# Kernel tuning notes

Measured on AMD Instinct MI355X. Metric: run time of the kernel, lower is better.

Reference implementation:

```python
import jax, jax.numpy as jnp
import numpy as np

B = 4096
N_ENTITY = 100000
N_USER = 10000
N_RELATION = 32
DIM = 64
N_ITER = 2
K = 16  # n_neighbors


def setup_inputs() -> dict:
    key = jax.random.key(0)
    ks = jax.random.split(key, 8)
    pairs = jax.random.randint(ks[0], (B, 2), 0, N_USER, dtype=jnp.int64 if jax.config.jax_enable_x64 else jnp.int32)
    adj_entity = jax.random.randint(ks[1], (N_ENTITY, K), 0, N_ENTITY)
    adj_relation = jax.random.randint(ks[2], (N_ENTITY, K), 0, N_RELATION)
    # xavier_uniform-style scale for embeddings
    def xavier(k, shape):
        limit = float(np.sqrt(6.0 / (shape[0] + shape[1])))
        return jax.random.uniform(k, shape, jnp.float32, -limit, limit)
    entity_emb = xavier(ks[3], (N_ENTITY, DIM))
    relation_emb = xavier(ks[4], (N_RELATION, DIM))
    user_emb = xavier(ks[5], (N_USER, DIM))
    W = xavier(ks[6], (DIM, DIM))
    b = jnp.zeros((DIM,), jnp.float32)
    return {"pairs": pairs, "adj_entity": adj_entity, "adj_relation": adj_relation,
            "entity_emb": entity_emb, "relation_emb": relation_emb,
            "user_emb": user_emb, "W": W, "b": b}


def reference(pairs, adj_entity, adj_relation, entity_emb, relation_emb, user_emb, W, b):
    n = pairs.shape[0]
    dim = entity_emb.shape[1]
    k = adj_entity.shape[1]
    users = pairs[:, 0]
    items = pairs[:, 1]

    # multi-hop neighbor expansion (mirrors get_neighbors)
    entities = [items]
    relations = []
    for i in range(N_ITER):
        entities.append(adj_entity[entities[i]].reshape(-1))
        relations.append(adj_relation[entities[i]].reshape(-1))

    u = user_emb[users]  # [B, D]
    ev = [entity_emb[entities[i]].reshape(n, -1, dim) for i in range(N_ITER + 1)]
    rv = [relation_emb[relations[i]].reshape(n, -1, dim) for i in range(N_ITER)]

    for l in range(N_ITER):
        nxt = []
        for i in range(N_ITER - l):
            r = rv[i].reshape(n, -1, k, dim)          # [B, M, K, D]
            scores = jnp.einsum('bd,bmkd->bmk', u, r) # user-relation attention
            attn = jax.nn.softmax(scores, axis=-1)[..., None]
            nbr = (attn * ev[i + 1].reshape(n, -1, k, dim)).sum(axis=-2)  # [B, M, D]
            x = ev[i].reshape(n, -1, dim) + nbr       # residual add
            h = x @ W.T + b                            # Linear(dim, dim)
            nxt.append(jnp.tanh(h) if l == N_ITER - 1 else jax.nn.relu(h))
        ev = nxt

    item_embeddings = ev[0].reshape(-1, dim)  # [B, D]
    return jax.nn.sigmoid(jnp.sum(u * item_embeddings, axis=1))
```

## Files before the change

kernel.cpp:

```cpp
#include <hip/hip_runtime.h>
#include <hip/hip_bf16.h>
#include <math.h>

#define DIM  64
#define KN   16
#define NREL 32
#define S8   0.00390625f

__device__ __forceinline__ float frcp(float x) { return __builtin_amdgcn_rcpf(x); }

__device__ __forceinline__ unsigned short f2bf(float f) {
    unsigned u = __float_as_uint(f);
    u = (u + 0x7fffu + ((u >> 16) & 1u)) >> 16;
    return (unsigned short)u;
}

typedef __attribute__((ext_vector_type(8))) short bfrag;
typedef __attribute__((ext_vector_type(4))) float f32x4;
typedef __attribute__((ext_vector_type(2))) float f32x2;

__global__ __launch_bounds__(256, 2) void we_kernel_mfma(
    const float* __restrict__ entity_emb,
    const float* __restrict__ W,
    const int* __restrict__ adjE,
    const int* __restrict__ adjR,
    unsigned char* __restrict__ WE8,
    int* __restrict__ adjP,
    int nRows)
{
    const int tid  = threadIdx.x;
    const int wave = tid >> 6;
    const int lane = tid & 63;
    const int c = lane & 15;
    const int g = lane >> 4;

    {
        const size_t nEntries = (size_t)nRows * KN;
        const size_t base = ((size_t)blockIdx.x * 256 + tid) * 8;
        if (base + 8 <= nEntries) {
            const int4* e4 = (const int4*)(adjE + base);
            const int4* r4 = (const int4*)(adjR + base);
            const int4 e0 = e4[0], e1v = e4[1];
            const int4 r0 = r4[0], r1v = r4[1];
            int4 p0, p1;
            p0.x = (e0.x << 5) | r0.x;  p0.y = (e0.y << 5) | r0.y;
            p0.z = (e0.z << 5) | r0.z;  p0.w = (e0.w << 5) | r0.w;
            p1.x = (e1v.x << 5) | r1v.x; p1.y = (e1v.y << 5) | r1v.y;
            p1.z = (e1v.z << 5) | r1v.z; p1.w = (e1v.w << 5) | r1v.w;
            ((int4*)(adjP + base))[0] = p0;
            ((int4*)(adjP + base))[1] = p1;
        } else if (base < nEntries) {
            for (size_t i = base; i < nEntries; ++i)
                adjP[i] = (adjE[i] << 5) | adjR[i];
        }
    }

    const int nTiles = (nRows + 15) >> 4;
    const int t0 = (blockIdx.x * 4 + wave) * 2;
    if (t0 >= nTiles) return;

    bfrag a[4][2];
    #pragma unroll
    for (int m = 0; m < 4; ++m) {
        #pragma unroll
        for (int ks = 0; ks < 2; ++ks) {
            const float4* ws = (const float4*)(W + (size_t)(16 * m + c) * DIM + 8 * g + 32 * ks);
            const float4 w0 = ws[0], w1 = ws[1];
            a[m][ks][0] = (short)f2bf(w0.x); a[m][ks][1] = (short)f2bf(w0.y);
            a[m][ks][2] = (short)f2bf(w0.z); a[m][ks][3] = (short)f2bf(w0.w);
            a[m][ks][4] = (short)f2bf(w1.x); a[m][ks][5] = (short)f2bf(w1.y);
            a[m][ks][6] = (short)f2bf(w1.z); a[m][ks][7] = (short)f2bf(w1.w);
        }
    }

    float4 pe[2][4];
    #pragma unroll
    for (int j = 0; j < 2; ++j) {
        const int t = (t0 + j < nTiles) ? (t0 + j) : 0;
        int row = 16 * t + c;
        if (row >= nRows) row = nRows - 1;
        const float4* src = (const float4*)(entity_emb + (size_t)row * DIM + 8 * g);
        pe[j][0] = src[0];
        pe[j][1] = src[1];
        pe[j][2] = src[8];
        pe[j][3] = src[9];
    }

    #pragma unroll
    for (int j = 0; j < 2; ++j) {
        const int t = t0 + j;
        if (t >= nTiles) continue;

        bfrag b0, b1;
        b0[0] = (short)f2bf(pe[j][0].x); b0[1] = (short)f2bf(pe[j][0].y);
        b0[2] = (short)f2bf(pe[j][0].z); b0[3] = (short)f2bf(pe[j][0].w);
        b0[4] = (short)f2bf(pe[j][1].x); b0[5] = (short)f2bf(pe[j][1].y);
        b0[6] = (short)f2bf(pe[j][1].z); b0[7] = (short)f2bf(pe[j][1].w);
        b1[0] = (short)f2bf(pe[j][2].x); b1[1] = (short)f2bf(pe[j][2].y);
        b1[2] = (short)f2bf(pe[j][2].z); b1[3] = (short)f2bf(pe[j][2].w);
        b1[4] = (short)f2bf(pe[j][3].x); b1[5] = (short)f2bf(pe[j][3].y);
        b1[6] = (short)f2bf(pe[j][3].z); b1[7] = (short)f2bf(pe[j][3].w);

        f32x4 acc[4];
        #pragma unroll
        for (int m = 0; m < 4; ++m) {
            f32x4 z = {0.f, 0.f, 0.f, 0.f};
            z = __builtin_amdgcn_mfma_f32_16x16x32_bf16(a[m][0], b0, z, 0, 0, 0);
            z = __builtin_amdgcn_mfma_f32_16x16x32_bf16(a[m][1], b1, z, 0, 0, 0);
            acc[m] = z;
        }

        const int erow = 16 * t + c;
        if (erow < nRows) {
            #pragma unroll
            for (int m = 0; m < 4; ++m) {
                int r8 = 0;
                r8 = __builtin_amdgcn_cvt_pk_fp8_f32(acc[m][0] * 256.f, acc[m][1] * 256.f, r8, false);
                r8 = __builtin_amdgcn_cvt_pk_fp8_f32(acc[m][2] * 256.f, acc[m][3] * 256.f, r8, true);
                *(unsigned*)(WE8 + (size_t)erow * DIM + 16 * m + 4 * g) = (unsigned)r8;
            }
        }
    }
}

__global__ __launch_bounds__(256, 4) void kgcn_main(
    const int* __restrict__ pairs,
    const int* __restrict__ adjP,
    const unsigned char* __restrict__ WE8,
    const float* __restrict__ relation_emb,
    const float* __restrict__ user_emb,
    const float* __restrict__ W,
    const float* __restrict__ bias,
    float* __restrict__ out,
    int nPairs)
{
    __shared__ float ev1_s[4][KN * DIM];
    __shared__ float xb_s[4][DIM];

    const int tid  = threadIdx.x;
    const int wave = tid >> 6;
    const int lane = tid & 63;
    const int p    = blockIdx.x * 4 + wave;
    if (p >= nPairs) return;

    float* ev1 = ev1_s[wave];
    float* xb  = xb_s[wave];

    const int qq = lane >> 4;
    const int c  = lane & 15;
    const int c4 = c * 4;

    const int user = pairs[2 * p + 0];
    const int item = pairs[2 * p + 1];

    const float4 b4 = *(const float4*)(bias + c4);
    const unsigned* W8q = (const unsigned*)WE8;

    int rk0 = 0, e1 = 0;
    if (lane < KN) {
        const int pk0 = adjP[(size_t)item * KN + lane];
        rk0 = pk0 & 31;
        e1  = pk0 >> 5;
    }

    float4 rr[8], ur[8];
    {
        const int r = lane >> 1, hlf = lane & 1;
        const float4* rel4 = (const float4*)(relation_emb + r * DIM + hlf * 32);
        const float4* u4   = (const float4*)(user_emb + (size_t)user * DIM + hlf * 32);
        #pragma unroll
        for (int j = 0; j < 8; ++j) { rr[j] = rel4[j]; ur[j] = u4[j]; }
    }

    const unsigned itemv8 = W8q[(size_t)item * 16 + c];
    unsigned h0v8[4];
    #pragma unroll
    for (int k = 0; k < 4; ++k) {
        const int e = __shfl(e1, qq * 4 + k);
        h0v8[k] = W8q[(size_t)(unsigned)e * 16 + c];
    }
    int rkA[4], ekA[4], gsA[4];
    #pragma unroll
    for (int s = 0; s < 4; ++s) {
        gsA[s] = __shfl(e1, 4 * s + qq);
        const int pk = adjP[(size_t)(unsigned)gsA[s] * KN + c];
        rkA[s] = pk & 31;
        ekA[s] = pk >> 5;
    }

    float acc;
    {
        float a0 = 0.f, a1 = 0.f;
        #pragma unroll
        for (int j = 0; j < 8; j += 2) {
            float4 a = rr[j],     b = ur[j];
            float4 cc = rr[j+1],  d = ur[j+1];
            a0 += a.x*b.x + a.y*b.y + a.z*b.z + a.w*b.w;
            a1 += cc.x*d.x + cc.y*d.y + cc.z*d.z + cc.w*d.w;
        }
        acc = a0 + a1;
        acc += __shfl_xor(acc, 1);
    }

    unsigned svA8[4];
    unsigned nvA[3][KN];
    #pragma unroll
    for (int s = 0; s < 3; ++s) {
        svA8[s] = W8q[(size_t)(unsigned)gsA[s] * 16 + c];
        #pragma unroll
        for (int k = 0; k < KN; ++k) {
            const int e = __shfl(ekA[s], qq * 16 + k);
            nvA[s][k] = W8q[(size_t)(unsigned)e * 16 + c];
        }
    }
    svA8[3] = W8q[(size_t)(unsigned)gsA[3] * 16 + c];

    auto softmax16 = [&](float s) -> float {
        float mx = s;
        mx = fmaxf(mx, __shfl_xor(mx, 1));
        mx = fmaxf(mx, __shfl_xor(mx, 2));
        mx = fmaxf(mx, __shfl_xor(mx, 4));
        mx = fmaxf(mx, __shfl_xor(mx, 8));
        float e = __expf(s - mx);
        float ss = e;
        ss += __shfl_xor(ss, 1);
        ss += __shfl_xor(ss, 2);
        ss += __shfl_xor(ss, 4);
        ss += __shfl_xor(ss, 8);
        return e * frcp(ss);
    };

    float wA[4];
    #pragma unroll
    for (int s = 0; s < 4; ++s) wA[s] = softmax16(__shfl(acc, rkA[s] << 1)) * S8;
    const float w0 = softmax16(__shfl(acc, rk0 << 1));

    {
        const f32x2 slo = __builtin_amdgcn_cvt_pk_f32_fp8(svA8[0], false);
        const f32x2 shi = __builtin_amdgcn_cvt_pk_f32_fp8(svA8[0], true);
        float ax = b4.x + S8 * slo.x;
        float ay = b4.y + S8 * slo.y;
        float az = b4.z + S8 * shi.x;
        float aw = b4.w + S8 * shi.y;
        #pragma unroll
        for (int k = 0; k < KN; ++k) {
            const float w = __shfl(wA[0], qq * 16 + k);
            const f32x2 lo = __builtin_amdgcn_cvt_pk_f32_fp8(nvA[0][k], false);
            const f32x2 hi = __builtin_amdgcn_cvt_pk_f32_fp8(nvA[0][k], true);
            ax += w * lo.x;
            ay += w * lo.y;
            az += w * hi.x;
            aw += w * hi.y;
        }
        *(float4*)&ev1[qq * DIM + c4] =
            make_float4(fmaxf(ax, 0.f), fmaxf(ay, 0.f), fmaxf(az, 0.f), fmaxf(aw, 0.f));
    }
    unsigned nv3[KN];
    #pragma unroll
    for (int k = 0; k < KN; ++k) {
        const int e = __shfl(ekA[3], qq * 16 + k);
        nv3[k] = W8q[(size_t)(unsigned)e * 16 + c];
    }
    #pragma unroll
    for (int s = 1; s < 3; ++s) {
        const f32x2 slo = __builtin_amdgcn_cvt_pk_f32_fp8(svA8[s], false);
        const f32x2 shi = __builtin_amdgcn_cvt_pk_f32_fp8(svA8[s], true);
        float ax = b4.x + S8 * slo.x;
        float ay = b4.y + S8 * slo.y;
        float az = b4.z + S8 * shi.x;
        float aw = b4.w + S8 * shi.y;
        #pragma unroll
        for (int k = 0; k < KN; ++k) {
            const float w = __shfl(wA[s], qq * 16 + k);
            const f32x2 lo = __builtin_amdgcn_cvt_pk_f32_fp8(nvA[s][k], false);
            const f32x2 hi = __builtin_amdgcn_cvt_pk_f32_fp8(nvA[s][k], true);
            ax += w * lo.x;
            ay += w * lo.y;
            az += w * hi.x;
            aw += w * hi.y;
        }
        *(float4*)&ev1[(4 * s + qq) * DIM + c4] =
            make_float4(fmaxf(ax, 0.f), fmaxf(ay, 0.f), fmaxf(az, 0.f), fmaxf(aw, 0.f));
    }
    {
        const f32x2 slo = __builtin_amdgcn_cvt_pk_f32_fp8(svA8[3], false);
        const f32x2 shi = __builtin_amdgcn_cvt_pk_f32_fp8(svA8[3], true);
        float ax = b4.x + S8 * slo.x;
        float ay = b4.y + S8 * slo.y;
        float az = b4.z + S8 * shi.x;
        float aw = b4.w + S8 * shi.y;
        #pragma unroll
        for (int k = 0; k < KN; ++k) {
            const float w = __shfl(wA[3], qq * 16 + k);
            const f32x2 lo = __builtin_amdgcn_cvt_pk_f32_fp8(nv3[k], false);
            const f32x2 hi = __builtin_amdgcn_cvt_pk_f32_fp8(nv3[k], true);
            ax += w * lo.x;
            ay += w * lo.y;
            az += w * hi.x;
            aw += w * hi.y;
        }
        *(float4*)&ev1[(12 + qq) * DIM + c4] =
            make_float4(fmaxf(ax, 0.f), fmaxf(ay, 0.f), fmaxf(az, 0.f), fmaxf(aw, 0.f));
    }

    float ax = 0.f, ay = 0.f, az = 0.f, aw = 0.f;
    #pragma unroll
    for (int k = 0; k < 4; ++k) {
        const float w = __shfl(w0, qq * 4 + k) * S8;
        const f32x2 lo = __builtin_amdgcn_cvt_pk_f32_fp8(h0v8[k], false);
        const f32x2 hi = __builtin_amdgcn_cvt_pk_f32_fp8(h0v8[k], true);
        ax += w * lo.x;
        ay += w * lo.y;
        az += w * hi.x;
        aw += w * hi.y;
    }
    ax += __shfl_xor(ax, 16); ay += __shfl_xor(ay, 16);
    az += __shfl_xor(az, 16); aw += __shfl_xor(aw, 16);
    ax += __shfl_xor(ax, 32); ay += __shfl_xor(ay, 32);
    az += __shfl_xor(az, 32); aw += __shfl_xor(aw, 32);
    {
        const f32x2 ilo = __builtin_amdgcn_cvt_pk_f32_fp8(itemv8, false);
        const f32x2 ihi = __builtin_amdgcn_cvt_pk_f32_fp8(itemv8, true);
        ax += S8 * ilo.x + b4.x;
        ay += S8 * ilo.y + b4.y;
        az += S8 * ihi.x + b4.z;
        aw += S8 * ihi.y + b4.w;
    }
    const float e0x = fmaxf(ax, 0.f), e0y = fmaxf(ay, 0.f);
    const float e0z = fmaxf(az, 0.f), e0w = fmaxf(aw, 0.f);

    asm volatile("s_waitcnt lgkmcnt(0)" ::: "memory");
    float sx = 0.f, sy = 0.f, sz = 0.f, sw = 0.f;
    #pragma unroll
    for (int k = 0; k < 4; ++k) {
        const int   kg = qq * 4 + k;
        const float w  = __shfl(w0, kg);
        float4 ev = *(const float4*)&ev1[kg * DIM + c4];
        sx += w * ev.x;
        sy += w * ev.y;
        sz += w * ev.z;
        sw += w * ev.w;
    }
    sx += __shfl_xor(sx, 16); sy += __shfl_xor(sy, 16);
    sz += __shfl_xor(sz, 16); sw += __shfl_xor(sw, 16);
    sx += __shfl_xor(sx, 32); sy += __shfl_xor(sy, 32);
    sz += __shfl_xor(sz, 32); sw += __shfl_xor(sw, 32);

    asm volatile("s_waitcnt lgkmcnt(0)" ::: "memory");
    if (qq == 0)
        *(float4*)&xb[c4] = make_float4(e0x + sx, e0y + sy, e0z + sz, e0w + sw);
    asm volatile("s_waitcnt lgkmcnt(0)" ::: "memory");
    float h0 = bias[lane], h1 = 0.f, h2 = 0.f, h3 = 0.f;
    {
        const float4* Wl  = (const float4*)(W + lane * DIM);
        const float4* xv4 = (const float4*)xb;
        #pragma unroll
        for (int j = 0; j < 16; j += 4) {
            float4 w0v = Wl[j],   x0v = xv4[j];
            float4 w1v = Wl[j+1], x1v = xv4[j+1];
            float4 w2v = Wl[j+2], x2v = xv4[j+2];
            float4 w3v = Wl[j+3], x3v = xv4[j+3];
            h0 += w0v.x*x0v.x + w0v.y*x0v.y + w0v.z*x0v.z + w0v.w*x0v.w;
            h1 += w1v.x*x1v.x + w1v.y*x1v.y + w1v.z*x1v.z + w1v.w*x1v.w;
            h2 += w2v.x*x2v.x + w2v.y*x2v.y + w2v.z*x2v.z + w2v.w*x2v.w;
            h3 += w3v.x*x3v.x + w3v.y*x3v.y + w3v.z*x3v.z + w3v.w*x3v.w;
        }
    }
    const float itemf = tanhf((h0 + h1) + (h2 + h3));

    float d = user_emb[(size_t)user * DIM + lane] * itemf;
    d += __shfl_xor(d, 1);
    d += __shfl_xor(d, 2);
    d += __shfl_xor(d, 4);
    d += __shfl_xor(d, 8);
    d += __shfl_xor(d, 16);
    d += __shfl_xor(d, 32);
    if (lane == 0) out[p] = 1.f / (1.f + expf(-d));
}

__global__ __launch_bounds__(256, 4) void kgcn_fallback(
    const int* __restrict__ pairs, const int* __restrict__ adj_entity,
    const int* __restrict__ adj_relation, const float* __restrict__ entity_emb,
    const float* __restrict__ relation_emb, const float* __restrict__ user_emb,
    const float* __restrict__ W, const float* __restrict__ bias,
    float* __restrict__ out, int nPairs)
{
    __shared__ float ev1_s[2][KN * DIM];
    __shared__ float xb_s[4][DIM];
    const int tid = threadIdx.x, wave = tid >> 6, lane = tid & 63;
    const int q = wave >> 1, half = wave & 1;
    int p = blockIdx.x * 2 + q;
    if (p >= nPairs) p = nPairs - 1;
    float* ev1 = ev1_s[q]; float* xb = xb_s[wave];
    const int user = pairs[2 * p + 0], item = pairs[2 * p + 1];
    const float bval = bias[lane];
    const float* emb_l = entity_emb + lane;
    const float4* W4 = (const float4*)(W + lane * DIM);
    int rk0 = 0, e1 = 0;
    if (lane < KN) {
        rk0 = adj_relation[(size_t)item * KN + lane];
        e1  = adj_entity[(size_t)item * KN + lane];
    }
    float acc;
    {
        const int r = lane >> 1, hlf = lane & 1;
        const float4* rel4 = (const float4*)(relation_emb + r * DIM + hlf * 32);
        const float4* u4 = (const float4*)(user_emb + (size_t)user * DIM + hlf * 32);
        float a0 = 0.f, a1 = 0.f;
        #pragma unroll
        for (int j = 0; j < 8; j += 2) {
            float4 a = rel4[j], b = u4[j], c = rel4[j+1], d = u4[j+1];
            a0 += a.x*b.x + a.y*b.y + a.z*b.z + a.w*b.w;
            a1 += c.x*d.x + c.y*d.y + c.z*d.z + c.w*d.w;
        }
        acc = a0 + a1; acc += __shfl_xor(acc, 1);
    }
    auto softmax16 = [&](float s) -> float {
        float mx = s;
        mx = fmaxf(mx, __shfl_xor(mx, 1)); mx = fmaxf(mx, __shfl_xor(mx, 2));
        mx = fmaxf(mx, __shfl_xor(mx, 4)); mx = fmaxf(mx, __shfl_xor(mx, 8));
        float e = __expf(s - mx);
        float ss = e;
        ss += __shfl_xor(ss, 1); ss += __shfl_xor(ss, 2);
        ss += __shfl_xor(ss, 4); ss += __shfl_xor(ss, 8);
        return e * frcp(ss);
    };
    auto matvec = [&](float xv) -> float {
        asm volatile("s_waitcnt lgkmcnt(0)" ::: "memory");
        xb[lane] = xv;
        asm volatile("s_waitcnt lgkmcnt(0)" ::: "memory");
        float h0 = bval, h1 = 0.f, h2 = 0.f, h3 = 0.f;
        const float4* xv4 = (const float4*)xb;
        #pragma unroll
        for (int j = 0; j < 16; j += 4) {
            float4 w0 = W4[j], x0 = xv4[j], w1 = W4[j+1], x1 = xv4[j+1];
            float4 w2 = W4[j+2], x2 = xv4[j+2], w3 = W4[j+3], x3 = xv4[j+3];
            h0 += w0.x*x0.x + w0.y*x0.y + w0.z*x0.z + w0.w*x0.w;
            h1 += w1.x*x1.x + w1.y*x1.y + w1.z*x1.z + w1.w*x1.w;
            h2 += w2.x*x2.x + w2.y*x2.y + w2.z*x2.z + w2.w*x2.w;
            h3 += w3.x*x3.x + w3.y*x3.y + w3.z*x3.z + w3.w*x3.w;
        }
        return (h0 + h1) + (h2 + h3);
    };
    auto gather = [&](int self, int ek, float w) -> float {
        float xa = emb_l[(size_t)(unsigned)self * DIM], xc = 0.f;
        #pragma unroll
        for (int k = 0; k < KN; k += 2) {
            const int e0i = __shfl(ek, k); const float f0 = __shfl(w, k);
            const int e1i = __shfl(ek, k + 1); const float f1 = __shfl(w, k + 1);
            xa += f0 * emb_l[(size_t)(unsigned)e0i * DIM];
            xc += f1 * emb_l[(size_t)(unsigned)e1i * DIM];
        }
        return xa + xc;
    };
    int rk_n = 0, ek_n = 0;
    {
        const int g0 = __shfl(e1, half * 8);
        if (lane < KN) {
            rk_n = adj_relation[(size_t)(unsigned)g0 * KN + lane];
            ek_n = adj_entity[(size_t)(unsigned)g0 * KN + lane];
        }
    }
    #pragma unroll 1
    for (int mi = 0; mi < 8; ++mi) {
        const int m = half * 8 + mi;
        const int g = __shfl(e1, m);
        const int rk = rk_n, ek = ek_n;
        if (mi + 1 < 8) {
            const int gn = __shfl(e1, m + 1);
            if (lane < KN) {
                rk_n = adj_relation[(size_t)(unsigned)gn * KN + lane];
                ek_n = adj_entity[(size_t)(unsigned)gn * KN + lane];
            }
        }
        const float w = softmax16(__shfl(acc, rk << 1));
        const float x = gather(g, ek, w);
        ev1[m * DIM + lane] = fmaxf(matvec(x), 0.f);
    }
    __syncthreads();
    if (half != 0) return;
    const float w0 = softmax16(__shfl(acc, rk0 << 1));
    const float x0 = gather(item, e1, w0);
    const float e0 = fmaxf(matvec(x0), 0.f);
    float xa = e0, xc = 0.f;
    #pragma unroll
    for (int k = 0; k < KN; k += 2) {
        xa += __shfl(w0, k) * ev1[k * DIM + lane];
        xc += __shfl(w0, k + 1) * ev1[(k + 1) * DIM + lane];
    }
    const float itemf = tanhf(matvec(xa + xc));
    float d = user_emb[(size_t)user * DIM + lane] * itemf;
    d += __shfl_xor(d, 1); d += __shfl_xor(d, 2); d += __shfl_xor(d, 4);
    d += __shfl_xor(d, 8); d += __shfl_xor(d, 16); d += __shfl_xor(d, 32);
    if (lane == 0) out[p] = 1.f / (1.f + expf(-d));
}

extern "C" void kernel_launch(void* const* d_in, const int* in_sizes, int n_in,
                              void* d_out, int out_size, void* d_ws, size_t ws_size,
                              hipStream_t stream) {
    const int*   pairs        = (const int*)d_in[0];
    const int*   adj_entity   = (const int*)d_in[1];
    const int*   adj_relation = (const int*)d_in[2];
    const float* entity_emb   = (const float*)d_in[3];
    const float* relation_emb = (const float*)d_in[4];
    const float* user_emb     = (const float*)d_in[5];
    const float* W            = (const float*)d_in[6];
    const float* b            = (const float*)d_in[7];
    float* out = (float*)d_out;

    const int nPairs = in_sizes[0] / 2;
    const int nEnt   = in_sizes[3] / DIM;
    const size_t w8Bytes   = (size_t)in_sizes[3] * sizeof(unsigned char);
    const size_t w8Aligned = (w8Bytes + 255) & ~(size_t)255;
    const size_t adjBytes  = (size_t)nEnt * KN * sizeof(int);

    if (ws_size >= w8Aligned + adjBytes) {
        unsigned char* WE8 = (unsigned char*)d_ws;
        int* adjP = (int*)((char*)d_ws + w8Aligned);
        const int nTiles = (nEnt + 15) >> 4;
        const int preBlocks = (nTiles + 7) / 8;
        we_kernel_mfma<<<preBlocks, 256, 0, stream>>>(entity_emb, W,
                                                      adj_entity, adj_relation,
                                                      WE8, adjP, nEnt);
        const int mainBlocks = (nPairs + 3) / 4;
        kgcn_main<<<mainBlocks, 256, 0, stream>>>(pairs, adjP,
                                                  WE8, relation_emb, user_emb,
                                                  W, b, out, nPairs);
    } else {
        const int nBlocks = (nPairs + 1) / 2;
        kgcn_fallback<<<nBlocks, 256, 0, stream>>>(pairs, adj_entity, adj_relation,
                                                   entity_emb, relation_emb, user_emb,
                                                   W, b, out, nPairs);
    }
}
```

Baseline: 125.5 us.

## Interleave FP8 projected embeddings and packed adjacency into one 128-byte record per entity

The separate FP8 W·E table and packed adjacency array are merged into a single array of 128-byte per-entity records: 64 bytes of FP8 embedding followed by 64 bytes of packed neighbor/relation indices. The main kernel then reads an entity's self embedding and its adjacency from the same record, which should improve locality for the hop-1 gathers. The preprocessing kernel now packs adjacency one row per thread and sizes its grid to cover the larger of the two tasks. The cost is that embedding-only gathers now touch a record stride twice as wide, which may waste cache-line capacity.

```diff
diff --git a/kernel.cpp b/kernel.cpp
--- a/kernel.cpp
+++ b/kernel.cpp
@@ -24,8 +24,7 @@
     const float* __restrict__ W,
     const int* __restrict__ adjE,
     const int* __restrict__ adjR,
-    unsigned char* __restrict__ WE8,
-    int* __restrict__ adjP,
+    unsigned char* __restrict__ rec,
     int nRows)
 {
     const int tid  = threadIdx.x;
@@ -35,23 +34,19 @@
     const int g = lane >> 4;
 
     {
-        const size_t nEntries = (size_t)nRows * KN;
-        const size_t base = ((size_t)blockIdx.x * 256 + tid) * 8;
-        if (base + 8 <= nEntries) {
-            const int4* e4 = (const int4*)(adjE + base);
-            const int4* r4 = (const int4*)(adjR + base);
-            const int4 e0 = e4[0], e1v = e4[1];
-            const int4 r0 = r4[0], r1v = r4[1];
-            int4 p0, p1;
-            p0.x = (e0.x << 5) | r0.x;  p0.y = (e0.y << 5) | r0.y;
-            p0.z = (e0.z << 5) | r0.z;  p0.w = (e0.w << 5) | r0.w;
-            p1.x = (e1v.x << 5) | r1v.x; p1.y = (e1v.y << 5) | r1v.y;
-            p1.z = (e1v.z << 5) | r1v.z; p1.w = (e1v.w << 5) | r1v.w;
-            ((int4*)(adjP + base))[0] = p0;
-            ((int4*)(adjP + base))[1] = p1;
-        } else if (base < nEntries) {
-            for (size_t i = base; i < nEntries; ++i)
-                adjP[i] = (adjE[i] << 5) | adjR[i];
+        const int r = blockIdx.x * 256 + tid;
+        if (r < nRows) {
+            const int4* e4 = (const int4*)(adjE + (size_t)r * KN);
+            const int4* r4 = (const int4*)(adjR + (size_t)r * KN);
+            int4* dst = (int4*)(rec + (size_t)r * 128 + 64);
+            #pragma unroll
+            for (int j = 0; j < 4; ++j) {
+                const int4 e = e4[j], rr = r4[j];
+                int4 pk;
+                pk.x = (e.x << 5) | rr.x;  pk.y = (e.y << 5) | rr.y;
+                pk.z = (e.z << 5) | rr.z;  pk.w = (e.w << 5) | rr.w;
+                dst[j] = pk;
+            }
         }
     }
 
@@ -117,7 +112,7 @@
                 int r8 = 0;
                 r8 = __builtin_amdgcn_cvt_pk_fp8_f32(acc[m][0] * 256.f, acc[m][1] * 256.f, r8, false);
                 r8 = __builtin_amdgcn_cvt_pk_fp8_f32(acc[m][2] * 256.f, acc[m][3] * 256.f, r8, true);
-                *(unsigned*)(WE8 + (size_t)erow * DIM + 16 * m + 4 * g) = (unsigned)r8;
+                *(unsigned*)(rec + (size_t)erow * 128 + 16 * m + 4 * g) = (unsigned)r8;
             }
         }
     }
@@ -125,8 +120,7 @@
 
 __global__ __launch_bounds__(256, 4) void kgcn_main(
     const int* __restrict__ pairs,
-    const int* __restrict__ adjP,
-    const unsigned char* __restrict__ WE8,
+    const unsigned* __restrict__ R,
     const float* __restrict__ relation_emb,
     const float* __restrict__ user_emb,
     const float* __restrict__ W,
@@ -154,11 +148,10 @@
     const int item = pairs[2 * p + 1];
 
     const float4 b4 = *(const float4*)(bias + c4);
-    const unsigned* W8q = (const unsigned*)WE8;
 
     int rk0 = 0, e1 = 0;
     if (lane < KN) {
-        const int pk0 = adjP[(size_t)item * KN + lane];
+        const int pk0 = (int)R[(size_t)item * 32 + 16 + lane];
         rk0 = pk0 & 31;
         e1  = pk0 >> 5;
     }
@@ -172,20 +165,23 @@
         for (int j = 0; j < 8; ++j) { rr[j] = rel4[j]; ur[j] = u4[j]; }
     }
 
-    const unsigned itemv8 = W8q[(size_t)item * 16 + c];
+    const unsigned itemv8 = R[(size_t)item * 32 + c];
     unsigned h0v8[4];
     #pragma unroll
     for (int k = 0; k < 4; ++k) {
         const int e = __shfl(e1, qq * 4 + k);
-        h0v8[k] = W8q[(size_t)(unsigned)e * 16 + c];
+        h0v8[k] = R[(size_t)(unsigned)e * 32 + c];
     }
     int rkA[4], ekA[4], gsA[4];
+    unsigned svA8[4];
     #pragma unroll
     for (int s = 0; s < 4; ++s) {
         gsA[s] = __shfl(e1, 4 * s + qq);
-        const int pk = adjP[(size_t)(unsigned)gsA[s] * KN + c];
+        const size_t base = (size_t)(unsigned)gsA[s] * 32;
+        const int pk = (int)R[base + 16 + c];
         rkA[s] = pk & 31;
         ekA[s] = pk >> 5;
+        svA8[s] = R[base + c];
     }
 
     float acc;
@@ -202,18 +198,15 @@
         acc += __shfl_xor(acc, 1);
     }
 
-    unsigned svA8[4];
     unsigned nvA[3][KN];
     #pragma unroll
     for (int s = 0; s < 3; ++s) {
-        svA8[s] = W8q[(size_t)(unsigned)gsA[s] * 16 + c];
         #pragma unroll
         for (int k = 0; k < KN; ++k) {
             const int e = __shfl(ekA[s], qq * 16 + k);
-            nvA[s][k] = W8q[(size_t)(unsigned)e * 16 + c];
-        }
-    }
-    svA8[3] = W8q[(size_t)(unsigned)gsA[3] * 16 + c];
+            nvA[s][k] = R[(size_t)(unsigned)e * 32 + c];
+        }
+    }
 
     auto softmax16 = [&](float s) -> float {
         float mx = s;
@@ -259,7 +252,7 @@
     #pragma unroll
     for (int k = 0; k < KN; ++k) {
         const int e = __shfl(ekA[3], qq * 16 + k);
-        nv3[k] = W8q[(size_t)(unsigned)e * 16 + c];
+        nv3[k] = R[(size_t)(unsigned)e * 32 + c];
     }
     #pragma unroll
     for (int s = 1; s < 3; ++s) {
@@ -510,21 +503,20 @@
 
     const int nPairs = in_sizes[0] / 2;
     const int nEnt   = in_sizes[3] / DIM;
-    const size_t w8Bytes   = (size_t)in_sizes[3] * sizeof(unsigned char);
-    const size_t w8Aligned = (w8Bytes + 255) & ~(size_t)255;
-    const size_t adjBytes  = (size_t)nEnt * KN * sizeof(int);
-
-    if (ws_size >= w8Aligned + adjBytes) {
-        unsigned char* WE8 = (unsigned char*)d_ws;
-        int* adjP = (int*)((char*)d_ws + w8Aligned);
+    const size_t recBytes = (size_t)nEnt * 128;
+
+    if (ws_size >= recBytes) {
+        unsigned char* rec = (unsigned char*)d_ws;
         const int nTiles = (nEnt + 15) >> 4;
-        const int preBlocks = (nTiles + 7) / 8;
+        int preBlocks = (nTiles + 7) / 8;
+        const int adjBlocks = (nEnt + 255) / 256;
+        if (adjBlocks > preBlocks) preBlocks = adjBlocks;
         we_kernel_mfma<<<preBlocks, 256, 0, stream>>>(entity_emb, W,
                                                       adj_entity, adj_relation,
-                                                      WE8, adjP, nEnt);
+                                                      rec, nEnt);
         const int mainBlocks = (nPairs + 3) / 4;
-        kgcn_main<<<mainBlocks, 256, 0, stream>>>(pairs, adjP,
-                                                  WE8, relation_emb, user_emb,
+        kgcn_main<<<mainBlocks, 256, 0, stream>>>(pairs, (const unsigned*)rec,
+                                                  relation_emb, user_emb,
                                                   W, b, out, nPairs);
     } else {
         const int nBlocks = (nPairs + 1) / 2;
```

Measured after the change: 127.9 us. Within noise of the previous version (+1.9%).
